# Kernel optimization log

Hardware: AMD Instinct MI355X
Metric: run time of the kernel (lower is better)

The kernel has to match this reference:

```python
import jax, jax.numpy as jnp
import numpy as np

EMBED_DIM = 1024
NUM_HEADS = 16
HEAD_DIM = EMBED_DIM // NUM_HEADS
SCALE = HEAD_DIM ** -0.5


def setup_inputs() -> dict:
    key = jax.random.key(0)
    ks = jax.random.split(key, 8)
    B, N = 4, 2048
    x = jax.random.normal(ks[0], (B, N, EMBED_DIM), dtype=jnp.float32)
    rope_cos = jax.random.uniform(ks[1], (N, HEAD_DIM), dtype=jnp.float32)
    rope_sin = jax.random.uniform(ks[2], (N, HEAD_DIM), dtype=jnp.float32)
    # Learned params (torch nn.Linear: y = x @ W.T + b); store W as [in, out]
    s_qkv = 1.0 / np.sqrt(EMBED_DIM)
    W_qkv = jax.random.uniform(ks[3], (EMBED_DIM, 3 * EMBED_DIM), dtype=jnp.float32, minval=-s_qkv, maxval=s_qkv)
    b_qkv = jax.random.uniform(ks[4], (3 * EMBED_DIM,), dtype=jnp.float32, minval=-s_qkv, maxval=s_qkv)
    W_proj = jax.random.uniform(ks[5], (EMBED_DIM, EMBED_DIM), dtype=jnp.float32, minval=-s_qkv, maxval=s_qkv)
    b_proj = jax.random.uniform(ks[6], (EMBED_DIM,), dtype=jnp.float32, minval=-s_qkv, maxval=s_qkv)
    return {"x": x, "rope_cos": rope_cos, "rope_sin": rope_sin,
            "W_qkv": W_qkv, "b_qkv": b_qkv, "W_proj": W_proj, "b_proj": b_proj}


def _rotate_half(t):
    t1, t2 = jnp.split(t, 2, axis=-1)
    return jnp.concatenate((-t2, t1), axis=-1)


def reference(x, rope_cos, rope_sin, W_qkv, b_qkv, W_proj, b_proj):
    B, N, D = x.shape
    qkv = x @ W_qkv + b_qkv                       # [B, N, 3D]
    qkv = qkv.reshape(B, N, 3, NUM_HEADS, HEAD_DIM)
    qkv = jnp.transpose(qkv, (2, 0, 3, 1, 4))     # [3, B, H, N, hd]
    q, k, v = qkv[0], qkv[1], qkv[2]
    cos = rope_cos[None, None]                    # [1, 1, N, hd]
    sin = rope_sin[None, None]
    q = q * cos + _rotate_half(q) * sin
    k = k * cos + _rotate_half(k) * sin
    attn = jnp.einsum('bhqd,bhkd->bhqk', q, k) * SCALE
    attn = jax.nn.softmax(attn, axis=-1)
    out = jnp.einsum('bhqk,bhkd->bhqd', attn, v)  # [B, H, N, hd]
    out = jnp.transpose(out, (0, 2, 1, 3)).reshape(B, N, D)
    return out @ W_proj + b_proj
```

## Files before the change

kernel.cpp:

```cpp
#include <hip/hip_runtime.h>
#include <stdint.h>

#define EMBED 1024
#define NHEAD 16
#define HD    64
#define SEQ   2048
#define BATCH 4

typedef __bf16 bf16x8 __attribute__((ext_vector_type(8)));
typedef __bf16 bf16x4 __attribute__((ext_vector_type(4)));
typedef float  f32x4  __attribute__((ext_vector_type(4)));
typedef unsigned int u32x2 __attribute__((ext_vector_type(2)));

#define GLB(p)  ((__attribute__((address_space(1))) unsigned int*)(p))
#define LDSP(p) ((__attribute__((address_space(3))) unsigned int*)(p))
#define MFMA(a,b,c) __builtin_amdgcn_mfma_f32_16x16x32_bf16(a,b,c,0,0,0)
#define EXP2(x) __builtin_amdgcn_exp2f(x)

#define QSCALE 0.18033688011112042f

__device__ __forceinline__ unsigned int f2bf(float f) {
    unsigned int u = __float_as_uint(f);
    return (u + 0x7FFFu + ((u >> 16) & 1u)) >> 16;
}
__device__ __forceinline__ unsigned int pack2(float a, float b) {
    return f2bf(a) | (f2bf(b) << 16);
}

__global__ void k_convert(const float* __restrict__ in, unsigned short* __restrict__ out, int n4) {
    int i = blockIdx.x * 256 + threadIdx.x;
    if (i >= n4) return;
    f32x4 v = ((const f32x4*)in)[i];
    u32x2 w = { pack2(v[0], v[1]), pack2(v[2], v[3]) };
    ((u32x2*)out)[i] = w;
}

__global__ void k_transpose(const float* __restrict__ in, unsigned short* __restrict__ out, int K, int C) {
    __shared__ float t[32][33];
    int c0 = blockIdx.x * 32, k0 = blockIdx.y * 32;
    int tid = threadIdx.x;
    #pragma unroll
    for (int i = 0; i < 4; i++) {
        int e = tid + i * 256;
        t[e >> 5][e & 31] = in[(size_t)(k0 + (e >> 5)) * C + c0 + (e & 31)];
    }
    __syncthreads();
    #pragma unroll
    for (int i = 0; i < 4; i++) {
        int e = tid + i * 256;
        int cl = e >> 5, kl = e & 31;
        out[(size_t)(c0 + cl) * K + k0 + kl] = (unsigned short)f2bf(t[kl][cl]);
    }
}

__global__ __launch_bounds__(256) void k_qkv(const unsigned short* __restrict__ xb,
    const unsigned short* __restrict__ wt, const float* __restrict__ bias,
    const float* __restrict__ rc, const float* __restrict__ rs,
    unsigned short* __restrict__ Qb, unsigned short* __restrict__ Kb, unsigned short* __restrict__ Vt)
{
    __shared__ unsigned short Al[128 * 32];
    __shared__ unsigned short Bl[128 * 32];
    const int tid = threadIdx.x;
    const int wave = tid >> 6, lane = tid & 63;
    const int l15 = lane & 15, l4 = lane >> 4;
    const int wr = wave >> 1, wc = wave & 1;
    const int tm = blockIdx.y * 128, tc = blockIdx.x * 128;

    const int srow = wave * 32 + (lane >> 2);
    const int scol = (lane & 3) * 8;
    const unsigned short* ga = xb + (size_t)(tm + srow) * EMBED + scol;
    const unsigned short* gb = wt + (size_t)(tc + srow) * EMBED + scol;

    f32x4 acc[4][4] = {};
    for (int k0 = 0; k0 < EMBED; k0 += 32) {
        __syncthreads();
        __builtin_amdgcn_global_load_lds(GLB(ga + k0),               LDSP(Al + wave * 1024),       16, 0, 0);
        __builtin_amdgcn_global_load_lds(GLB(ga + k0 + 16 * EMBED),  LDSP(Al + wave * 1024 + 512), 16, 0, 0);
        __builtin_amdgcn_global_load_lds(GLB(gb + k0),               LDSP(Bl + wave * 1024),       16, 0, 0);
        __builtin_amdgcn_global_load_lds(GLB(gb + k0 + 16 * EMBED),  LDSP(Bl + wave * 1024 + 512), 16, 0, 0);
        __syncthreads();
        bf16x8 af[4], bfr[4];
        #pragma unroll
        for (int m = 0; m < 4; m++) af[m]  = *(const bf16x8*)&Al[(wr * 64 + m * 16 + l15) * 32 + l4 * 8];
        #pragma unroll
        for (int n = 0; n < 4; n++) bfr[n] = *(const bf16x8*)&Bl[(wc * 64 + n * 16 + l15) * 32 + l4 * 8];
        #pragma unroll
        for (int m = 0; m < 4; m++)
            #pragma unroll
            for (int n = 0; n < 4; n++)
                acc[m][n] = MFMA(af[m], bfr[n], acc[m][n]);
    }

    const int cb = tc + wc * 64;
    const int s = cb >> 10;
    const int h = (cb >> 6) & 15;
    if (s < 2) {
        #pragma unroll
        for (int m = 0; m < 4; m++)
            #pragma unroll
            for (int j = 0; j < 4; j++) {
                int row = tm + wr * 64 + m * 16 + l4 * 4 + j;
                int b = row >> 11, pos = row & (SEQ - 1);
                float v[4];
                #pragma unroll
                for (int n = 0; n < 4; n++) v[n] = acc[m][n][j] + bias[cb + n * 16 + l15];
                float o[4];
                #pragma unroll
                for (int p = 0; p < 2; p++) {
                    int d1 = p * 16 + l15;
                    float c1 = rc[pos * HD + d1],      s1 = rs[pos * HD + d1];
                    float c2 = rc[pos * HD + d1 + 32], s2 = rs[pos * HD + d1 + 32];
                    o[p]     = v[p] * c1     - v[p + 2] * s1;
                    o[p + 2] = v[p + 2] * c2 + v[p] * s2;
                }
                float mul = (s == 0) ? QSCALE : 1.0f;
                unsigned short* dst = (s == 0 ? Qb : Kb) + ((size_t)(b * NHEAD + h) * SEQ + pos) * HD;
                #pragma unroll
                for (int n = 0; n < 4; n++) dst[n * 16 + l15] = (unsigned short)f2bf(o[n] * mul);
            }
    } else {
        #pragma unroll
        for (int m = 0; m < 4; m++) {
            int row0 = tm + wr * 64 + m * 16 + l4 * 4;
            int b = row0 >> 11, pos0 = row0 & (SEQ - 1);
            #pragma unroll
            for (int n = 0; n < 4; n++) {
                float bb = bias[cb + n * 16 + l15];
                u32x2 w = { pack2(acc[m][n][0] + bb, acc[m][n][1] + bb),
                            pack2(acc[m][n][2] + bb, acc[m][n][3] + bb) };
                *(u32x2*)(Vt + ((size_t)(b * NHEAD + h) * HD + n * 16 + l15) * SEQ + pos0) = w;
            }
        }
    }
}

__global__ __launch_bounds__(256) void k_attn(const unsigned short* __restrict__ Qb,
    const unsigned short* __restrict__ Kb, const unsigned short* __restrict__ Vt,
    unsigned short* __restrict__ O)
{
    __shared__ unsigned short Kl[2][64 * 64];
    __shared__ unsigned short Vl[2][64 * 64];
    __shared__ unsigned short Pl[128 * 64];
    const int tid = threadIdx.x, wave = tid >> 6, lane = tid & 63;
    const int l15 = lane & 15, l4 = lane >> 4;
    const int bh = blockIdx.y;
    const int b = bh >> 4, h = bh & 15;
    const int q0 = blockIdx.x * 128 + wave * 32;

    const unsigned short* Qg = Qb + ((size_t)bh * SEQ + q0) * HD;
    bf16x8 qf[2][2];
    #pragma unroll
    for (int qb = 0; qb < 2; qb++)
        #pragma unroll
        for (int ds = 0; ds < 2; ds++)
            qf[qb][ds] = *(const bf16x8*)(Qg + (qb * 16 + l15) * HD + ds * 32 + l4 * 8);

    const int srow = lane >> 3;
    const int selem = ((lane & 7) * 8) ^ ((srow & 7) * 8);
    const unsigned short* kg = Kb + (size_t)bh * SEQ * HD + (size_t)(wave * 16 + srow) * HD + selem;
    const unsigned short* vg = Vt + (size_t)bh * HD * SEQ + (size_t)(wave * 16 + srow) * SEQ + selem;

#define ISSUE(kt_, bi_) do { \
    __builtin_amdgcn_global_load_lds(GLB(kg + (size_t)(kt_) * HD),       LDSP(&Kl[bi_][0] + wave * 1024),       16, 0, 0); \
    __builtin_amdgcn_global_load_lds(GLB(kg + (size_t)((kt_) + 8) * HD), LDSP(&Kl[bi_][0] + wave * 1024 + 512), 16, 0, 0); \
    __builtin_amdgcn_global_load_lds(GLB(vg + (kt_)),                    LDSP(&Vl[bi_][0] + wave * 1024),       16, 0, 0); \
    __builtin_amdgcn_global_load_lds(GLB(vg + 8 * SEQ + (kt_)),          LDSP(&Vl[bi_][0] + wave * 1024 + 512), 16, 0, 0); \
} while (0)

    f32x4 accO[2][4] = {};
    float mst[2] = { -1e30f, -1e30f }, lst[2] = { 0.f, 0.f };

    ISSUE(0, 0);

    for (int kt = 0; kt < SEQ; kt += 64) {
        const int cur = (kt >> 6) & 1;
        __builtin_amdgcn_s_barrier();
        if (kt + 64 < SEQ) {
            ISSUE(kt + 64, cur ^ 1);
            asm volatile("s_waitcnt vmcnt(4)" ::: "memory");
        } else {
            asm volatile("s_waitcnt vmcnt(0)" ::: "memory");
        }
        __builtin_amdgcn_sched_barrier(0);

        const unsigned short* Klc = &Kl[cur][0];
        const unsigned short* Vlc = &Vl[cur][0];

        f32x4 sacc[2][4] = {};
        __builtin_amdgcn_s_setprio(1);
        #pragma unroll
        for (int ds = 0; ds < 2; ds++)
            #pragma unroll
            for (int kb = 0; kb < 4; kb++) {
                int krow = kb * 16 + l15;
                bf16x8 kf = *(const bf16x8*)((const char*)Klc + krow * 128 + ((ds * 64 + l4 * 16) ^ ((krow & 7) << 4)));
                sacc[0][kb] = MFMA(kf, qf[0][ds], sacc[0][kb]);
                sacc[1][kb] = MFMA(kf, qf[1][ds], sacc[1][kb]);
            }
        __builtin_amdgcn_s_setprio(0);

        #pragma unroll
        for (int qb = 0; qb < 2; qb++) {
            float pm = -1e30f;
            #pragma unroll
            for (int kb = 0; kb < 4; kb++)
                #pragma unroll
                for (int r = 0; r < 4; r++) pm = fmaxf(pm, sacc[qb][kb][r]);
            pm = fmaxf(pm, __shfl_xor(pm, 16));
            pm = fmaxf(pm, __shfl_xor(pm, 32));
            bool skip = __all(pm <= mst[qb] + 8.f);
            float mnew = skip ? mst[qb] : fmaxf(mst[qb], pm);
            float ls = 0.f;
            bf16x4 pw[4];
            #pragma unroll
            for (int kb = 0; kb < 4; kb++) {
                float p0 = EXP2(sacc[qb][kb][0] - mnew);
                float p1 = EXP2(sacc[qb][kb][1] - mnew);
                float p2 = EXP2(sacc[qb][kb][2] - mnew);
                float p3 = EXP2(sacc[qb][kb][3] - mnew);
                ls += (p0 + p1) + (p2 + p3);
                pw[kb][0] = (__bf16)p0; pw[kb][1] = (__bf16)p1;
                pw[kb][2] = (__bf16)p2; pw[kb][3] = (__bf16)p3;
            }
            ls += __shfl_xor(ls, 16);
            ls += __shfl_xor(ls, 32);
            if (skip) {
                lst[qb] += ls;
            } else {
                float corr = EXP2(mst[qb] - mnew);
                mst[qb] = mnew;
                lst[qb] = lst[qb] * corr + ls;
                #pragma unroll
                for (int db = 0; db < 4; db++) accO[qb][db] *= corr;
            }
            int prow = wave * 32 + qb * 16 + l15;
            #pragma unroll
            for (int kb = 0; kb < 4; kb++) {
                int pbyte = prow * 128 + ((kb * 32 + l4 * 8) ^ ((prow & 7) << 4));
                *(bf16x4*)((char*)Pl + pbyte) = pw[kb];
            }
        }

        __builtin_amdgcn_s_setprio(1);
        #pragma unroll
        for (int ds = 0; ds < 2; ds++) {
            int prow0 = wave * 32 + l15, prow1 = prow0 + 16;
            bf16x8 pf0 = *(const bf16x8*)((const char*)Pl + prow0 * 128 + ((ds * 64 + l4 * 16) ^ ((prow0 & 7) << 4)));
            bf16x8 pf1 = *(const bf16x8*)((const char*)Pl + prow1 * 128 + ((ds * 64 + l4 * 16) ^ ((prow1 & 7) << 4)));
            #pragma unroll
            for (int db = 0; db < 4; db++) {
                int vrow = db * 16 + l15;
                bf16x8 vf = *(const bf16x8*)((const char*)Vlc + vrow * 128 + ((ds * 64 + l4 * 16) ^ ((vrow & 7) << 4)));
                accO[0][db] = MFMA(vf, pf0, accO[0][db]);
                accO[1][db] = MFMA(vf, pf1, accO[1][db]);
            }
        }
        __builtin_amdgcn_s_setprio(0);
    }
#undef ISSUE

    #pragma unroll
    for (int qb = 0; qb < 2; qb++) {
        float inv = 1.f / lst[qb];
        int tok = q0 + qb * 16 + l15;
        size_t rowo = ((size_t)b * SEQ + tok) * EMBED + h * HD;
        #pragma unroll
        for (int db = 0; db < 4; db++) {
            u32x2 w = { pack2(accO[qb][db][0] * inv, accO[qb][db][1] * inv),
                        pack2(accO[qb][db][2] * inv, accO[qb][db][3] * inv) };
            *(u32x2*)(O + rowo + db * 16 + l4 * 4) = w;
        }
    }
}

__global__ __launch_bounds__(256) void k_proj(const unsigned short* __restrict__ A,
    const unsigned short* __restrict__ wt, const float* __restrict__ bias, float* __restrict__ out)
{
    __shared__ unsigned short Al[128 * 32];
    __shared__ unsigned short Bl[128 * 32];
    const int tid = threadIdx.x;
    const int wave = tid >> 6, lane = tid & 63;
    const int l15 = lane & 15, l4 = lane >> 4;
    const int wr = wave >> 1, wc = wave & 1;
    const int tm = blockIdx.y * 128, tc = blockIdx.x * 128;

    const int srow = wave * 32 + (lane >> 2);
    const int scol = (lane & 3) * 8;
    const unsigned short* ga = A  + (size_t)(tm + srow) * EMBED + scol;
    const unsigned short* gb = wt + (size_t)(tc + srow) * EMBED + scol;

    f32x4 acc[4][4] = {};
    for (int k0 = 0; k0 < EMBED; k0 += 32) {
        __syncthreads();
        __builtin_amdgcn_global_load_lds(GLB(ga + k0),              LDSP(Al + wave * 1024),       16, 0, 0);
        __builtin_amdgcn_global_load_lds(GLB(ga + k0 + 16 * EMBED), LDSP(Al + wave * 1024 + 512), 16, 0, 0);
        __builtin_amdgcn_global_load_lds(GLB(gb + k0),              LDSP(Bl + wave * 1024),       16, 0, 0);
        __builtin_amdgcn_global_load_lds(GLB(gb + k0 + 16 * EMBED), LDSP(Bl + wave * 1024 + 512), 16, 0, 0);
        __syncthreads();
        bf16x8 af[4], bfr[4];
        #pragma unroll
        for (int m = 0; m < 4; m++) af[m]  = *(const bf16x8*)&Al[(wr * 64 + m * 16 + l15) * 32 + l4 * 8];
        #pragma unroll
        for (int n = 0; n < 4; n++) bfr[n] = *(const bf16x8*)&Bl[(wc * 64 + n * 16 + l15) * 32 + l4 * 8];
        #pragma unroll
        for (int m = 0; m < 4; m++)
            #pragma unroll
            for (int n = 0; n < 4; n++)
                acc[m][n] = MFMA(af[m], bfr[n], acc[m][n]);
    }

    #pragma unroll
    for (int m = 0; m < 4; m++)
        #pragma unroll
        for (int j = 0; j < 4; j++) {
            int row = tm + wr * 64 + m * 16 + l4 * 4 + j;
            #pragma unroll
            for (int n = 0; n < 4; n++) {
                int col = tc + wc * 64 + n * 16 + l15;
                out[(size_t)row * EMBED + col] = acc[m][n][j] + bias[col];
            }
        }
}

extern "C" void kernel_launch(void* const* d_in, const int* in_sizes, int n_in,
                              void* d_out, int out_size, void* d_ws, size_t ws_size,
                              hipStream_t stream) {
    const float* x     = (const float*)d_in[0];
    const float* rc    = (const float*)d_in[1];
    const float* rs    = (const float*)d_in[2];
    const float* Wqkv  = (const float*)d_in[3];
    const float* bqkv  = (const float*)d_in[4];
    const float* Wproj = (const float*)d_in[5];
    const float* bproj = (const float*)d_in[6];
    char* ws = (char*)d_ws;
    unsigned short* xb  = (unsigned short*)(ws);
    unsigned short* wqt = (unsigned short*)(ws + 16777216);
    unsigned short* wpt = (unsigned short*)(ws + 23068672);
    unsigned short* Qb  = (unsigned short*)(ws + 25165824);
    unsigned short* Kb  = (unsigned short*)(ws + 41943040);
    unsigned short* Vt  = (unsigned short*)(ws + 58720256);
    float* outp = (float*)d_out;

    k_convert  <<<8192, 256, 0, stream>>>(x, xb, 2097152);
    k_transpose<<<dim3(96, 32), 256, 0, stream>>>(Wqkv, wqt, 1024, 3072);
    k_transpose<<<dim3(32, 32), 256, 0, stream>>>(Wproj, wpt, 1024, 1024);
    k_qkv      <<<dim3(24, 64), 256, 0, stream>>>(xb, wqt, bqkv, rc, rs, Qb, Kb, Vt);
    k_attn     <<<dim3(16, 64), 256, 0, stream>>>(Qb, Kb, Vt, xb);
    k_proj     <<<dim3(8, 64),  256, 0, stream>>>(xb, wpt, bproj, outp);
}
```

Before: 342.1 us.

## Keep softmax P in registers via permlane swaps instead of LDS round-trip

The attention kernel now rearranges the bf16 probability tile across lanes with permlane32/permlane16 swaps, so it can be fed straight to the PV MFMA as the B operand. This removes the Pl shared-memory buffer and its write/read traffic, and frees LDS that may allow higher occupancy. The K/V prefetch wait also changes: it waits for all outstanding loads before the barrier and then issues the next tile, so the prefetch now overlaps the current tile's compute but the wait no longer overlaps with the issue. Packing now uses the compiler's bf16 conversion (cvtpk) instead of manual bit tricks.

```diff
diff --git a/kernel.cpp b/kernel.cpp
--- a/kernel.cpp
+++ b/kernel.cpp
@@ -8,9 +8,10 @@
 #define BATCH 4
 
 typedef __bf16 bf16x8 __attribute__((ext_vector_type(8)));
-typedef __bf16 bf16x4 __attribute__((ext_vector_type(4)));
+typedef __bf16 bf16x2t __attribute__((ext_vector_type(2)));
 typedef float  f32x4  __attribute__((ext_vector_type(4)));
 typedef unsigned int u32x2 __attribute__((ext_vector_type(2)));
+typedef unsigned int u32x4 __attribute__((ext_vector_type(4)));
 
 #define GLB(p)  ((__attribute__((address_space(1))) unsigned int*)(p))
 #define LDSP(p) ((__attribute__((address_space(3))) unsigned int*)(p))
@@ -25,6 +26,41 @@
 }
 __device__ __forceinline__ unsigned int pack2(float a, float b) {
     return f2bf(a) | (f2bf(b) << 16);
+}
+__device__ __forceinline__ unsigned int cvtpk(float lo, float hi) {
+    bf16x2t w; w[0] = (__bf16)lo; w[1] = (__bf16)hi;
+    return __builtin_bit_cast(unsigned int, w);
+}
+
+__device__ __forceinline__ void pswap32(unsigned int &a, unsigned int &b) {
+#if __has_builtin(__builtin_amdgcn_permlane32_swap)
+    u32x2 r = __builtin_amdgcn_permlane32_swap(a, b, false, false);
+    a = r[0]; b = r[1];
+#else
+    unsigned int sa = (unsigned int)__shfl_xor((int)a, 32);
+    unsigned int sb = (unsigned int)__shfl_xor((int)b, 32);
+    bool hi = (threadIdx.x & 32) != 0;
+    unsigned int na = hi ? sb : a;
+    unsigned int nb = hi ? b : sa;
+    a = na; b = nb;
+#endif
+}
+__device__ __forceinline__ void pswap16(unsigned int &a, unsigned int &b) {
+#if __has_builtin(__builtin_amdgcn_permlane16_swap)
+    u32x2 r = __builtin_amdgcn_permlane16_swap(a, b, false, false);
+    a = r[0]; b = r[1];
+#else
+    unsigned int sa = (unsigned int)__shfl_xor((int)a, 16);
+    unsigned int sb = (unsigned int)__shfl_xor((int)b, 16);
+    bool oddq = (threadIdx.x & 16) != 0;
+    unsigned int na = oddq ? sb : a;
+    unsigned int nb = oddq ? b : sa;
+    a = na; b = nb;
+#endif
+}
+__device__ __forceinline__ void pswap_q(unsigned int &a, unsigned int &b) {
+    pswap32(a, b);
+    pswap16(a, b);
 }
 
 __global__ void k_convert(const float* __restrict__ in, unsigned short* __restrict__ out, int n4) {
@@ -140,7 +176,6 @@
 {
     __shared__ unsigned short Kl[2][64 * 64];
     __shared__ unsigned short Vl[2][64 * 64];
-    __shared__ unsigned short Pl[128 * 64];
     const int tid = threadIdx.x, wave = tid >> 6, lane = tid & 63;
     const int l15 = lane & 15, l4 = lane >> 4;
     const int bh = blockIdx.y;
@@ -174,13 +209,9 @@
 
     for (int kt = 0; kt < SEQ; kt += 64) {
         const int cur = (kt >> 6) & 1;
+        asm volatile("s_waitcnt vmcnt(0)" ::: "memory");
         __builtin_amdgcn_s_barrier();
-        if (kt + 64 < SEQ) {
-            ISSUE(kt + 64, cur ^ 1);
-            asm volatile("s_waitcnt vmcnt(4)" ::: "memory");
-        } else {
-            asm volatile("s_waitcnt vmcnt(0)" ::: "memory");
-        }
+        if (kt + 64 < SEQ) ISSUE(kt + 64, cur ^ 1);
         __builtin_amdgcn_sched_barrier(0);
 
         const unsigned short* Klc = &Kl[cur][0];
@@ -199,6 +230,7 @@
             }
         __builtin_amdgcn_s_setprio(0);
 
+        bf16x8 pf[2][2];
         #pragma unroll
         for (int qb = 0; qb < 2; qb++) {
             float pm = -1e30f;
@@ -211,7 +243,7 @@
             bool skip = __all(pm <= mst[qb] + 8.f);
             float mnew = skip ? mst[qb] : fmaxf(mst[qb], pm);
             float ls = 0.f;
-            bf16x4 pw[4];
+            unsigned int w[4][2];
             #pragma unroll
             for (int kb = 0; kb < 4; kb++) {
                 float p0 = EXP2(sacc[qb][kb][0] - mnew);
@@ -219,8 +251,8 @@
                 float p2 = EXP2(sacc[qb][kb][2] - mnew);
                 float p3 = EXP2(sacc[qb][kb][3] - mnew);
                 ls += (p0 + p1) + (p2 + p3);
-                pw[kb][0] = (__bf16)p0; pw[kb][1] = (__bf16)p1;
-                pw[kb][2] = (__bf16)p2; pw[kb][3] = (__bf16)p3;
+                w[kb][0] = cvtpk(p0, p1);
+                w[kb][1] = cvtpk(p2, p3);
             }
             ls += __shfl_xor(ls, 16);
             ls += __shfl_xor(ls, 32);
@@ -233,28 +265,26 @@
                 #pragma unroll
                 for (int db = 0; db < 4; db++) accO[qb][db] *= corr;
             }
-            int prow = wave * 32 + qb * 16 + l15;
-            #pragma unroll
-            for (int kb = 0; kb < 4; kb++) {
-                int pbyte = prow * 128 + ((kb * 32 + l4 * 8) ^ ((prow & 7) << 4));
-                *(bf16x4*)((char*)Pl + pbyte) = pw[kb];
-            }
+            pswap_q(w[0][0], w[1][0]);
+            pswap_q(w[0][1], w[1][1]);
+            pswap_q(w[2][0], w[3][0]);
+            pswap_q(w[2][1], w[3][1]);
+            u32x4 f0 = { w[0][0], w[0][1], w[1][0], w[1][1] };
+            u32x4 f1 = { w[2][0], w[2][1], w[3][0], w[3][1] };
+            pf[qb][0] = __builtin_bit_cast(bf16x8, f0);
+            pf[qb][1] = __builtin_bit_cast(bf16x8, f1);
         }
 
         __builtin_amdgcn_s_setprio(1);
         #pragma unroll
-        for (int ds = 0; ds < 2; ds++) {
-            int prow0 = wave * 32 + l15, prow1 = prow0 + 16;
-            bf16x8 pf0 = *(const bf16x8*)((const char*)Pl + prow0 * 128 + ((ds * 64 + l4 * 16) ^ ((prow0 & 7) << 4)));
-            bf16x8 pf1 = *(const bf16x8*)((const char*)Pl + prow1 * 128 + ((ds * 64 + l4 * 16) ^ ((prow1 & 7) << 4)));
+        for (int ds = 0; ds < 2; ds++)
             #pragma unroll
             for (int db = 0; db < 4; db++) {
                 int vrow = db * 16 + l15;
                 bf16x8 vf = *(const bf16x8*)((const char*)Vlc + vrow * 128 + ((ds * 64 + l4 * 16) ^ ((vrow & 7) << 4)));
-                accO[0][db] = MFMA(vf, pf0, accO[0][db]);
-                accO[1][db] = MFMA(vf, pf1, accO[1][db]);
-            }
-        }
+                accO[0][db] = MFMA(vf, pf[0][ds], accO[0][db]);
+                accO[1][db] = MFMA(vf, pf[1][ds], accO[1][db]);
+            }
         __builtin_amdgcn_s_setprio(0);
     }
 #undef ISSUE
```

Result: no change. 339.6 us (-0.7%).
